# Kernel optimization log

Measured on AMD Instinct MI355X. Metric: run time of the kernel, lower is better.

The kernel has to match this reference:

```python
import jax, jax.numpy as jnp
import numpy as np

DMODEL = 1024
N_MAMBAS = 4
D_INNER = 2 * DMODEL          # expand = 2
D_STATE = 16                  # mamba_ssm default
D_CONV = 4                    # mamba_ssm default
DT_RANK = DMODEL // 16        # ceil(d_model/16) = 64


def setup_inputs() -> dict:
    key = jax.random.key(0)
    ks = jax.random.split(key, 8)
    B, L, n = 2, 4096, N_MAMBAS
    f32 = jnp.float32
    x = jax.random.normal(ks[0], (B, L, DMODEL), f32)
    in_w = jax.random.normal(ks[1], (n, 2 * D_INNER, DMODEL), f32) * 0.02
    conv_w = jax.random.normal(ks[2], (n, D_INNER, D_CONV), f32) * 0.1
    conv_b = jnp.zeros((n, D_INNER), f32)
    xproj_w = jax.random.normal(ks[3], (n, DT_RANK + 2 * D_STATE, D_INNER), f32) * 0.02
    dt_w = jax.random.normal(ks[4], (n, D_INNER, DT_RANK), f32) * 0.02
    # softplus-inverse of dt_init ~ 0.01 (mamba-style dt bias init)
    dt_b = jnp.log(jnp.expm1(jnp.full((n, D_INNER), 0.01, f32)))
    # S4D-real init: A_log = log(1..d_state)
    A_log = jnp.log(jnp.broadcast_to(jnp.arange(1, D_STATE + 1, dtype=f32), (n, D_INNER, D_STATE)))
    D_skip = jnp.ones((n, D_INNER), f32)
    out_w = jax.random.normal(ks[5], (n, DMODEL, D_INNER), f32) * 0.02
    return dict(x=x, in_w=in_w, conv_w=conv_w, conv_b=conv_b, xproj_w=xproj_w,
                dt_w=dt_w, dt_b=dt_b, A_log=A_log, D_skip=D_skip, out_w=out_w)


def _mamba(x, in_w, conv_w, conv_b, xproj_w, dt_w, dt_b, A_log, D_skip, out_w):
    # x: (B, Lc, D)
    Bb = x.shape[0]
    xz = jnp.einsum('bld,ed->ble', x, in_w)                 # (B, Lc, 2*D_INNER)
    xi, z = jnp.split(xz, 2, axis=-1)
    # causal depthwise conv over time
    xc = jnp.transpose(xi, (0, 2, 1))                       # (B, D_INNER, Lc)
    xc = jax.lax.conv_general_dilated(xc, conv_w[:, None, :], (1,),
                                      [(D_CONV - 1, 0)], feature_group_count=D_INNER)
    xi = jax.nn.silu(jnp.transpose(xc + conv_b[None, :, None], (0, 2, 1)))  # (B, Lc, D_INNER)
    proj = jnp.einsum('bld,ed->ble', xi, xproj_w)           # (B, Lc, DT_RANK + 2*D_STATE)
    dt = proj[..., :DT_RANK]
    Bm = proj[..., DT_RANK:DT_RANK + D_STATE]
    Cm = proj[..., DT_RANK + D_STATE:]
    dt = jax.nn.softplus(jnp.einsum('blr,dr->bld', dt, dt_w) + dt_b)  # (B, Lc, D_INNER)
    A = -jnp.exp(A_log)                                     # (D_INNER, D_STATE)

    def step(h, inp):
        dt_t, B_t, C_t, x_t = inp                           # (B,Di),(B,Ds),(B,Ds),(B,Di)
        dA = jnp.exp(dt_t[:, :, None] * A)                  # (B, Di, Ds)
        h = dA * h + dt_t[:, :, None] * B_t[:, None, :] * x_t[:, :, None]
        return h, jnp.einsum('bds,bs->bd', h, C_t)

    h0 = jnp.zeros((Bb, D_INNER, D_STATE), x.dtype)
    xs_t = (jnp.swapaxes(dt, 0, 1), jnp.swapaxes(Bm, 0, 1),
            jnp.swapaxes(Cm, 0, 1), jnp.swapaxes(xi, 0, 1))
    _, ys = jax.lax.scan(step, h0, xs_t)                    # (Lc, B, D_INNER)
    y = jnp.swapaxes(ys, 0, 1) + xi * D_skip                # (B, Lc, D_INNER)
    y = y * jax.nn.silu(z)
    return jnp.einsum('ble,de->bld', y, out_w)              # (B, Lc, D)


def reference(x, in_w, conv_w, conv_b, xproj_w, dt_w, dt_b, A_log, D_skip, out_w):
    B, L, D = x.shape
    n = N_MAMBAS
    # strided slices x[:, i::n] == reshape(B, L//n, n, D)[:, :, i]
    xs = jnp.transpose(x.reshape(B, L // n, n, D), (2, 0, 1, 3))   # (n, B, Lc, D)
    ys = jax.vmap(_mamba)(xs, in_w, conv_w, conv_b, xproj_w,
                          dt_w, dt_b, A_log, D_skip, out_w)        # (n, B, Lc, D)
    # torch.cat(dim=1) concatenates per-mamba outputs block-wise along seq
    return jnp.transpose(ys, (1, 0, 2, 3)).reshape(B, L, D)
```

## Files before the change

kernel.cpp:

```cpp
#include <hip/hip_runtime.h>
#include <math.h>

#define DM   1024
#define DI   2048
#define DSn  16
#define DTR  64
#define PW   96
#define LS   1024
#define NCH  16
#define CL   64
#define XKS  4

typedef unsigned short u16;
typedef unsigned int   u32;
typedef __attribute__((ext_vector_type(8))) short bf16x8;
typedef __attribute__((ext_vector_type(8))) unsigned short u16x8;
typedef __attribute__((ext_vector_type(4))) float f32x4;

__device__ __forceinline__ void bar_lds() {
  asm volatile("s_waitcnt lgkmcnt(0)\n\ts_barrier" ::: "memory");
}

__device__ __forceinline__ void split2(float f, u16& hi, u16& lo) {
  union { float f; unsigned int u; } v; v.f = f;
  hi = (u16)(v.u >> 16);
  union { unsigned int u; float f; } w; w.u = v.u & 0xffff0000u;
  union { float f; unsigned int u; } r; r.f = f - w.f;
  lo = (u16)(r.u >> 16);
}

template<int ROWS>
__device__ __forceinline__ bf16x8 frag(const u16* T, int l4, int row) {
  return *(const bf16x8*)&T[(l4 * ROWS + row) * 8];
}

template<int ROWS>
__device__ __forceinline__ void stage16f(const float* a, u16* Th, u16* Tl, int ra, int half) {
  #pragma unroll
  for (int q = 0; q < 2; ++q) {
    u16x8 vh, vl;
    #pragma unroll
    for (int c = 0; c < 8; ++c) {
      u16 h_, l_;
      split2(a[q * 8 + c], h_, l_);
      vh[c] = h_; vl[c] = l_;
    }
    const int slot = ((half * 2 + q) * ROWS + ra) * 8;
    *(u16x8*)&Th[slot] = vh;
    *(u16x8*)&Tl[slot] = vl;
  }
}

__global__ __launch_bounds__(256) void k_split_x(
    const float* __restrict__ x, u16* __restrict__ xh, u16* __restrict__ xl, int ib0)
{
  const int idx = blockIdx.x * 256 + threadIdx.x;
  const int t = idx >> 8, kq = (idx & 255) * 4;
  const int gt = ib0 * 1024 + t;
  const int j = gt & (LS - 1), ib = gt >> 10;
  const int i = ib >> 1, bb = ib & 1;
  const float4 v = *(const float4*)&x[(size_t)(bb * 4096 + j * 4 + i) * DM + kq];
  ushort4 vh, vl;
  split2(v.x, vh.x, vl.x); split2(v.y, vh.y, vl.y);
  split2(v.z, vh.z, vl.z); split2(v.w, vh.w, vl.w);
  *(ushort4*)&xh[(size_t)t * DM + kq] = vh;
  *(ushort4*)&xl[(size_t)t * DM + kq] = vl;
}

#define KGP 2064
__global__ __launch_bounds__(512, 2) void k_inproj(
    const u16* __restrict__ xh, const u16* __restrict__ xl,
    const float* __restrict__ inwf,
    float* __restrict__ xz, int ib0, int swz)
{
  __shared__ __align__(16) u16 L[2][4][4][KGP];
  const int tid = threadIdx.x;
  int mblk, nblk;
  if (swz) {
    const int o = blockIdx.x;
    const int xcd = o & 7, within = o >> 3;
    mblk = xcd * 4 + (within & 3);
    nblk = within >> 2;
  } else {
    mblk = blockIdx.x; nblk = blockIdx.y;
  }
  const int m0 = mblk << 8, n0 = nblk << 8;
  const int ib = ib0 + (m0 >> 10);
  const int il = (ib >> 1) - (ib0 >> 1);
  const int ra = tid >> 1, half = tid & 1;
  const u16* Aph = xh + (size_t)(m0 + ra) * DM + half * 16;
  const u16* Apl = xl + (size_t)(m0 + ra) * DM + half * 16;
  const float* Bpf = inwf + ((size_t)il * 4096 + n0 + ra) * DM + half * 16;
  const int w = tid >> 6, lane = tid & 63;
  const int wr = w >> 2, wc = w & 3;
  const int l15 = lane & 15, l4 = lane >> 4;

  f32x4 acc[8][4];
  #pragma unroll
  for (int a_ = 0; a_ < 8; ++a_)
    #pragma unroll
    for (int b_ = 0; b_ < 4; ++b_) acc[a_][b_] = (f32x4)(0.f);

  u16x8 ah2[2], al2[2];
  float br[16];

  auto LOADG = [&](int kt) {
    const int k0 = kt * 32;
    ah2[0] = *(const u16x8*)(Aph + k0);
    ah2[1] = *(const u16x8*)(Aph + k0 + 8);
    al2[0] = *(const u16x8*)(Apl + k0);
    al2[1] = *(const u16x8*)(Apl + k0 + 8);
    *(f32x4*)&br[0]  = *(const f32x4*)(Bpf + k0);
    *(f32x4*)&br[4]  = *(const f32x4*)(Bpf + k0 + 4);
    *(f32x4*)&br[8]  = *(const f32x4*)(Bpf + k0 + 8);
    *(f32x4*)&br[12] = *(const f32x4*)(Bpf + k0 + 12);
  };
  auto STORE = [&](int b) {
    #pragma unroll
    for (int q = 0; q < 2; ++q) {
      const int kg = half * 2 + q;
      *(u16x8*)&L[b][0][kg][ra * 8] = ah2[q];
      *(u16x8*)&L[b][1][kg][ra * 8] = al2[q];
      u16x8 vh, vl;
      #pragma unroll
      for (int c = 0; c < 8; ++c) {
        u16 h_, l_;
        split2(br[q * 8 + c], h_, l_);
        vh[c] = h_; vl[c] = l_;
      }
      *(u16x8*)&L[b][2][kg][ra * 8] = vh;
      *(u16x8*)&L[b][3][kg][ra * 8] = vl;
    }
  };
  auto COMPUTE = [&](int b) {
    bf16x8 bh[4], bl[4];
    #pragma unroll
    for (int nf = 0; nf < 4; ++nf) {
      const int col = wc * 64 + nf * 16 + l15;
      bh[nf] = *(const bf16x8*)&L[b][2][l4][col * 8];
      bl[nf] = *(const bf16x8*)&L[b][3][l4][col * 8];
    }
    #pragma unroll
    for (int mf = 0; mf < 8; ++mf) {
      const int row = wr * 128 + mf * 16 + l15;
      bf16x8 ah = *(const bf16x8*)&L[b][0][l4][row * 8];
      bf16x8 al = *(const bf16x8*)&L[b][1][l4][row * 8];
      #pragma unroll
      for (int nf = 0; nf < 4; ++nf) {
        acc[mf][nf] = __builtin_amdgcn_mfma_f32_16x16x32_bf16(ah, bh[nf], acc[mf][nf], 0, 0, 0);
        acc[mf][nf] = __builtin_amdgcn_mfma_f32_16x16x32_bf16(ah, bl[nf], acc[mf][nf], 0, 0, 0);
        acc[mf][nf] = __builtin_amdgcn_mfma_f32_16x16x32_bf16(al, bh[nf], acc[mf][nf], 0, 0, 0);
      }
    }
  };

  const int nk = DM / 32;
  LOADG(0);
  STORE(0);
  if (nk > 1) LOADG(1);
  bar_lds();
  for (int kt = 0; kt < nk; ++kt) {
    const int c = kt & 1;
    if (kt + 1 < nk) STORE(c ^ 1);
    if (kt + 2 < nk) LOADG(kt + 2);
    COMPUTE(c);
    bar_lds();
  }

  #pragma unroll
  for (int mf = 0; mf < 8; ++mf) {
    const int row = m0 + wr * 128 + mf * 16 + l4 * 4;
    #pragma unroll
    for (int nf = 0; nf < 4; ++nf) {
      const int col = n0 + wc * 64 + nf * 16 + l15;
      #pragma unroll
      for (int r = 0; r < 4; ++r)
        xz[(size_t)(row + r) * (2 * DI) + col] = acc[mf][nf][r];
    }
  }
}

__global__ __launch_bounds__(256) void k_conv(
    const float* __restrict__ xz, const float* __restrict__ convw,
    const float* __restrict__ convb, float* __restrict__ xib,
    int ib0, int ntok)
{
  const int idx = blockIdx.x * 256 + threadIdx.x;
  if (idx >= ntok * (DI / 4)) return;
  const int t = idx / (DI / 4);
  const int c = (idx - t * (DI / 4)) * 4;
  const int j = t & (LS - 1);
  const int i = (ib0 + (t >> 10)) >> 1;
  float4 acc = *(const float4*)&convb[(size_t)i * DI + c];
  float4 wt[4];
  #pragma unroll
  for (int q = 0; q < 4; ++q)
    wt[q] = *(const float4*)&convw[((size_t)i * DI + c + q) * 4];
  #pragma unroll
  for (int k = 0; k < 4; ++k) {
    const int j2 = j + k - 3;
    if (j2 >= 0) {
      const float4 v = *(const float4*)&xz[(size_t)(t + k - 3) * (2 * DI) + c];
      acc.x = fmaf(v.x, ((const float*)&wt[0])[k], acc.x);
      acc.y = fmaf(v.y, ((const float*)&wt[1])[k], acc.y);
      acc.z = fmaf(v.z, ((const float*)&wt[2])[k], acc.z);
      acc.w = fmaf(v.w, ((const float*)&wt[3])[k], acc.w);
    }
  }
  float4 o;
  o.x = acc.x / (1.f + __expf(-acc.x));
  o.y = acc.y / (1.f + __expf(-acc.y));
  o.z = acc.z / (1.f + __expf(-acc.z));
  o.w = acc.w / (1.f + __expf(-acc.w));
  *(float4*)&xib[(size_t)t * DI + c] = o;
}

__global__ __launch_bounds__(256) void k_xproj_part(
    const float* __restrict__ xif, const float* __restrict__ xwf,
    float* __restrict__ Pp, int ib0, int ntok)
{
  __shared__ __align__(16) u16 Ah[2][4*64*8], Al[2][4*64*8];
  __shared__ __align__(16) u16 Bh[2][4*96*8], Bl[2][4*96*8];
  const int tid = threadIdx.x;
  const int m0 = blockIdx.x << 6;
  const int ks = blockIdx.y;
  const int kbase = ks * (DI / XKS);
  const int ib = ib0 + (m0 >> 10);
  const int il = (ib >> 1) - (ib0 >> 1);
  const int ra = tid >> 1, half = tid & 1;
  const bool hasA = (tid < 128);
  const bool hasB = (tid < 192);
  const float* Apf = xif + (size_t)(m0 + ra) * DI + kbase + half * 16;
  const float* Bpf = xwf + ((size_t)il * PW + ra) * DI + kbase + half * 16;
  const int w = tid >> 6, lane = tid & 63;
  const int l15 = lane & 15, l4 = lane >> 4;

  f32x4 acc[6];
  #pragma unroll
  for (int b_ = 0; b_ < 6; ++b_) acc[b_] = (f32x4)(0.f);

  float ar[16], br[16];
  auto LOADAB = [&](int kt) {
    const int k0 = kt * 32;
    if (hasA) {
      #pragma unroll
      for (int q = 0; q < 4; ++q) *(f32x4*)&ar[q*4] = *(const f32x4*)(Apf + k0 + q*4);
    }
    if (hasB) {
      #pragma unroll
      for (int q = 0; q < 4; ++q) *(f32x4*)&br[q*4] = *(const f32x4*)(Bpf + k0 + q*4);
    }
  };
  auto STORE = [&](int b) {
    if (hasA) stage16f<64>(ar, Ah[b], Al[b], ra, half);
    if (hasB) stage16f<96>(br, Bh[b], Bl[b], ra, half);
  };
  auto COMPUTE = [&](int b) {
    const int arow = w * 16 + l15;
    bf16x8 ah = frag<64>(Ah[b], l4, arow);
    bf16x8 al = frag<64>(Al[b], l4, arow);
    #pragma unroll
    for (int nf = 0; nf < 6; ++nf) {
      const int col = nf * 16 + l15;
      bf16x8 bh = frag<96>(Bh[b], l4, col);
      bf16x8 bl = frag<96>(Bl[b], l4, col);
      acc[nf] = __builtin_amdgcn_mfma_f32_16x16x32_bf16(ah, bh, acc[nf], 0, 0, 0);
      acc[nf] = __builtin_amdgcn_mfma_f32_16x16x32_bf16(ah, bl, acc[nf], 0, 0, 0);
      acc[nf] = __builtin_amdgcn_mfma_f32_16x16x32_bf16(al, bh, acc[nf], 0, 0, 0);
    }
  };

  const int nk = (DI / XKS) / 32;
  LOADAB(0);
  STORE(0);
  LOADAB(1);
  bar_lds();
  for (int kt = 0; kt < nk; ++kt) {
    const int c = kt & 1;
    if (kt + 1 < nk) STORE(c ^ 1);
    if (kt + 2 < nk) LOADAB(kt + 2);
    COMPUTE(c);
    bar_lds();
  }

  float* outp = Pp + (size_t)ks * ntok * PW;
  const int row = m0 + w * 16 + l4 * 4;
  #pragma unroll
  for (int nf = 0; nf < 6; ++nf) {
    const int col = nf * 16 + l15;
    #pragma unroll
    for (int r = 0; r < 4; ++r)
      outp[(size_t)(row + r) * PW + col] = acc[nf][r];
  }
}

__global__ __launch_bounds__(256) void k_xproj_red(
    const float* __restrict__ Pp, float* __restrict__ projb, int ntok)
{
  const int idx = blockIdx.x * 256 + threadIdx.x;
  if (idx >= ntok * PW) return;
  const size_t plane = (size_t)ntok * PW;
  float s = 0.f;
  #pragma unroll
  for (int ks = 0; ks < XKS; ++ks) s += Pp[(size_t)ks * plane + idx];
  projb[idx] = s;
}

__global__ __launch_bounds__(256) void k_dtproj(
    const float* __restrict__ proj, const float* __restrict__ dtw,
    const float* __restrict__ dtbias, float* __restrict__ dtout,
    int dstride, int ib0)
{
  __shared__ __align__(16) u16 Ah[8*128*8], Al[8*128*8];
  __shared__ __align__(16) u16 Bh[8*128*8], Bl[8*128*8];
  const int tid = threadIdx.x;
  const int n0 = blockIdx.x << 7;
  const int m0 = blockIdx.y << 7;
  const int ib = ib0 + (m0 >> 10);
  const int i  = ib >> 1;
  const int ra = tid >> 1, half = tid & 1;
  const float* Ap = proj + (size_t)(m0 + ra) * PW + half * 32;
  const float* Bp = dtw + ((size_t)i * DI + n0 + ra) * DTR + half * 32;
  const int w = tid >> 6, lane = tid & 63;
  const int wr = w >> 1, wc = w & 1;
  const int l15 = lane & 15, l4 = lane >> 4;

  {
    float av[32], bv[32];
    #pragma unroll
    for (int q = 0; q < 8; ++q) *(f32x4*)&av[q*4] = *(const f32x4*)(Ap + q*4);
    #pragma unroll
    for (int q = 0; q < 8; ++q) *(f32x4*)&bv[q*4] = *(const f32x4*)(Bp + q*4);
    #pragma unroll
    for (int q = 0; q < 4; ++q) {
      u16x8 vh, vl, wh, wl;
      #pragma unroll
      for (int c = 0; c < 8; ++c) {
        u16 h_, l_;
        split2(av[q*8+c], h_, l_); vh[c] = h_; vl[c] = l_;
        split2(bv[q*8+c], h_, l_); wh[c] = h_; wl[c] = l_;
      }
      const int slot = ((half*4 + q) * 128 + ra) * 8;
      *(u16x8*)&Ah[slot] = vh; *(u16x8*)&Al[slot] = vl;
      *(u16x8*)&Bh[slot] = wh; *(u16x8*)&Bl[slot] = wl;
    }
  }
  __syncthreads();

  f32x4 acc[4][4];
  #pragma unroll
  for (int a_ = 0; a_ < 4; ++a_)
    #pragma unroll
    for (int b_ = 0; b_ < 4; ++b_) acc[a_][b_] = (f32x4)(0.f);

  #pragma unroll
  for (int c = 0; c < 2; ++c) {
    bf16x8 bh[4], bl[4];
    #pragma unroll
    for (int nf = 0; nf < 4; ++nf) {
      const int col = wc * 64 + nf * 16 + l15;
      bh[nf] = *(const bf16x8*)&Bh[((4*c + l4) * 128 + col) * 8];
      bl[nf] = *(const bf16x8*)&Bl[((4*c + l4) * 128 + col) * 8];
    }
    #pragma unroll
    for (int mf = 0; mf < 4; ++mf) {
      const int row = wr * 64 + mf * 16 + l15;
      bf16x8 ah = *(const bf16x8*)&Ah[((4*c + l4) * 128 + row) * 8];
      bf16x8 al = *(const bf16x8*)&Al[((4*c + l4) * 128 + row) * 8];
      #pragma unroll
      for (int nf = 0; nf < 4; ++nf) {
        acc[mf][nf] = __builtin_amdgcn_mfma_f32_16x16x32_bf16(ah, bh[nf], acc[mf][nf], 0, 0, 0);
        acc[mf][nf] = __builtin_amdgcn_mfma_f32_16x16x32_bf16(ah, bl[nf], acc[mf][nf], 0, 0, 0);
        acc[mf][nf] = __builtin_amdgcn_mfma_f32_16x16x32_bf16(al, bh[nf], acc[mf][nf], 0, 0, 0);
      }
    }
  }

  #pragma unroll
  for (int nf = 0; nf < 4; ++nf) {
    const int col = n0 + wc * 64 + nf * 16 + l15;
    const float bias = dtbias[(size_t)i * DI + col];
    #pragma unroll
    for (int mf = 0; mf < 4; ++mf) {
      const int t0 = m0 + wr * 64 + mf * 16 + l4 * 4;
      #pragma unroll
      for (int r = 0; r < 4; ++r) {
        const float u = acc[mf][nf][r] + bias;
        const float sp = (u > 20.f) ? u : log1pf(__expf(u));
        dtout[(size_t)(t0 + r) * dstride + col] = sp;
      }
    }
  }
}

__global__ __launch_bounds__(256) void k_scan_part(
    const float* __restrict__ projb, const float* dtp, int dstride,
    const float* __restrict__ xib, const float* __restrict__ A_log,
    float* __restrict__ Pbuf, float* __restrict__ Hbuf, int ib0)
{
  const int d = blockIdx.x * 256 + threadIdx.x;
  const int ch = blockIdx.y, lib = blockIdx.z;
  const int i = (ib0 + lib) >> 1;
  const size_t gd = (size_t)i * DI + d;
  __shared__ float bs[CL][DSn];
  const size_t trow = (size_t)lib * LS + (size_t)ch * CL;
  for (int p = threadIdx.x; p < CL * DSn; p += 256) {
    const int jj = p >> 4, ss = p & 15;
    bs[jj][ss] = projb[(trow + jj) * PW + DTR + ss];
  }
  float A[DSn], P[DSn], h[DSn];
  #pragma unroll
  for (int s = 0; s < DSn; ++s) {
    A[s] = -__expf(A_log[gd * DSn + s]);
    P[s] = 1.f; h[s] = 0.f;
  }
  __syncthreads();
  float dt_c = dtp[trow * dstride + d];
  float xi_c = xib[trow * DI + d];
  for (int j = 0; j < CL; ++j) {
    float dt_n = 0.f, xi_n = 0.f;
    if (j + 1 < CL) {
      dt_n = dtp[(trow + j + 1) * dstride + d];
      xi_n = xib[(trow + j + 1) * DI + d];
    }
    const float dx = dt_c * xi_c;
    #pragma unroll
    for (int s = 0; s < DSn; ++s) {
      const float dA = __expf(dt_c * A[s]);
      P[s] *= dA;
      h[s] = fmaf(dA, h[s], dx * bs[j][s]);
    }
    dt_c = dt_n; xi_c = xi_n;
  }
  const size_t base = ((size_t)(lib * NCH + ch) * DSn) * DI + d;
  #pragma unroll
  for (int s = 0; s < DSn; ++s) {
    Pbuf[base + (size_t)s * DI] = P[s];
    Hbuf[base + (size_t)s * DI] = h[s];
  }
}

__global__ __launch_bounds__(256) void k_scan_mid(
    float* __restrict__ Pbuf, const float* __restrict__ Hbuf, int nib)
{
  const int idx = blockIdx.x * 256 + threadIdx.x;
  if (idx >= nib * DSn * DI) return;
  const int d = idx & (DI - 1);
  const int s = (idx >> 11) & 15;
  const int lib = idx >> 15;
  const size_t stride = (size_t)DSn * DI;
  const size_t base = ((size_t)lib * NCH * DSn + s) * DI + d;
  float carry = 0.f;
  for (int c = 0; c < NCH; ++c) {
    const size_t o = base + (size_t)c * stride;
    const float p = Pbuf[o];
    const float hl = Hbuf[o];
    Pbuf[o] = carry;
    carry = fmaf(p, carry, hl);
  }
}

__global__ __launch_bounds__(256) void k_scan_full(
    const float* __restrict__ projb, const float* dtp, int dstride,
    float* xibio, const float* xzz,
    const float* __restrict__ A_log, const float* __restrict__ D_skip,
    const float* __restrict__ Pbuf, int ib0)
{
  const int d = blockIdx.x * 256 + threadIdx.x;
  const int ch = blockIdx.y, lib = blockIdx.z;
  const int i = (ib0 + lib) >> 1;
  const size_t gd = (size_t)i * DI + d;
  __shared__ float bs[CL][2 * DSn];
  const size_t trow = (size_t)lib * LS + (size_t)ch * CL;
  for (int p = threadIdx.x; p < CL * 2 * DSn; p += 256) {
    const int jj = p >> 5, ss = p & 31;
    bs[jj][ss] = projb[(trow + jj) * PW + DTR + ss];
  }
  float A[DSn], h[DSn];
  const size_t hbase = ((size_t)(lib * NCH + ch) * DSn) * DI + d;
  #pragma unroll
  for (int s = 0; s < DSn; ++s) {
    A[s] = -__expf(A_log[gd * DSn + s]);
    h[s] = Pbuf[hbase + (size_t)s * DI];
  }
  const float Dsk = D_skip[gd];
  __syncthreads();
  float dt_c = dtp[trow * dstride + d];
  float xi_c = xibio[trow * DI + d];
  float z_c  = xzz[trow * (2 * DI) + DI + d];
  for (int j = 0; j < CL; ++j) {
    float dt_n = 0.f, xi_n = 0.f, z_n = 0.f;
    if (j + 1 < CL) {
      dt_n = dtp[(trow + j + 1) * dstride + d];
      xi_n = xibio[(trow + j + 1) * DI + d];
      z_n  = xzz[(trow + j + 1) * (2 * DI) + DI + d];
    }
    const float dx = dt_c * xi_c;
    float y = 0.f;
    #pragma unroll
    for (int s = 0; s < DSn; ++s) {
      const float dA = __expf(dt_c * A[s]);
      h[s] = fmaf(dA, h[s], dx * bs[j][s]);
      y = fmaf(h[s], bs[j][DSn + s], y);
    }
    const float sz = z_c / (1.f + __expf(-z_c));
    const float val = (y + xi_c * Dsk) * sz;
    u16 vh, vl;
    split2(val, vh, vl);
    ((u32*)xibio)[(trow + j) * DI + d] = ((u32)vh << 16) | (u32)vl;
    dt_c = dt_n; xi_c = xi_n; z_c = z_n;
  }
}

__global__ __launch_bounds__(256) void k_outproj(
    const u32* __restrict__ ybp, const float* __restrict__ owf,
    float* __restrict__ out, int ib0)
{
  __shared__ __align__(16) u16 Ah[2][4*128*8], Al[2][4*128*8];
  __shared__ __align__(16) u16 Bh[2][4*128*8], Bl[2][4*128*8];
  const int tid = threadIdx.x;
  const int m0 = blockIdx.x << 7;
  const int n0 = blockIdx.y << 7;
  const int ib = ib0 + (m0 >> 10);
  const int i = ib >> 1, bb = ib & 1;
  const int il = i - (ib0 >> 1);
  const int ra = tid >> 1, half = tid & 1;
  const u32* Ap = ybp + (size_t)(m0 + ra) * DI + half * 16;
  const int rb = tid >> 1;
  const float* Bpf = owf + ((size_t)il * DM + n0 + rb) * DI + half * 16;
  const int w = tid >> 6, lane = tid & 63;
  const int wr = w >> 1, wc = w & 1;
  const int l15 = lane & 15, l4 = lane >> 4;

  f32x4 acc[4][4];
  #pragma unroll
  for (int a_ = 0; a_ < 4; ++a_)
    #pragma unroll
    for (int b_ = 0; b_ < 4; ++b_) acc[a_][b_] = (f32x4)(0.f);

  uint4 qa[4];
  float br[16];
  auto LOADG = [&](int kt) {
    const int k0 = kt * 32;
    qa[0] = *(const uint4*)(Ap + k0);     qa[1] = *(const uint4*)(Ap + k0 + 4);
    qa[2] = *(const uint4*)(Ap + k0 + 8); qa[3] = *(const uint4*)(Ap + k0 + 12);
    #pragma unroll
    for (int q = 0; q < 4; ++q) *(f32x4*)&br[q*4] = *(const f32x4*)(Bpf + k0 + q*4);
  };
  auto STORE = [&](int b) {
    #pragma unroll
    for (int g = 0; g < 2; ++g) {
      const u32 e[8] = { qa[2*g].x, qa[2*g].y, qa[2*g].z, qa[2*g].w,
                         qa[2*g+1].x, qa[2*g+1].y, qa[2*g+1].z, qa[2*g+1].w };
      u16x8 vh, vl;
      #pragma unroll
      for (int c = 0; c < 8; ++c) { vh[c] = (u16)(e[c] >> 16); vl[c] = (u16)(e[c] & 0xffffu); }
      const int slot = ((half*2+g)*128 + ra)*8;
      *(u16x8*)&Ah[b][slot] = vh;
      *(u16x8*)&Al[b][slot] = vl;
    }
    stage16f<128>(br, Bh[b], Bl[b], rb, half);
  };
  auto COMPUTE = [&](int b) {
    bf16x8 ah[4], al[4];
    #pragma unroll
    for (int mf = 0; mf < 4; ++mf) {
      const int row = wr * 64 + mf * 16 + l15;
      ah[mf] = frag<128>(Ah[b], l4, row);
      al[mf] = frag<128>(Al[b], l4, row);
    }
    #pragma unroll
    for (int nf = 0; nf < 4; ++nf) {
      const int col = wc * 64 + nf * 16 + l15;
      bf16x8 bh = frag<128>(Bh[b], l4, col);
      bf16x8 bl = frag<128>(Bl[b], l4, col);
      #pragma unroll
      for (int mf = 0; mf < 4; ++mf) {
        acc[mf][nf] = __builtin_amdgcn_mfma_f32_16x16x32_bf16(ah[mf], bh, acc[mf][nf], 0, 0, 0);
        acc[mf][nf] = __builtin_amdgcn_mfma_f32_16x16x32_bf16(ah[mf], bl, acc[mf][nf], 0, 0, 0);
        acc[mf][nf] = __builtin_amdgcn_mfma_f32_16x16x32_bf16(al[mf], bh, acc[mf][nf], 0, 0, 0);
      }
    }
  };

  const int nk = DI / 32;
  LOADG(0);
  STORE(0);
  LOADG(1);
  bar_lds();
  for (int kt = 0; kt < nk; ++kt) {
    const int c = kt & 1;
    if (kt + 1 < nk) STORE(c ^ 1);
    if (kt + 2 < nk) LOADG(kt + 2);
    COMPUTE(c);
    bar_lds();
  }

  #pragma unroll
  for (int mf = 0; mf < 4; ++mf) {
    const int t0 = m0 + wr * 64 + mf * 16 + l4 * 4;
    #pragma unroll
    for (int nf = 0; nf < 4; ++nf) {
      const int col = n0 + wc * 64 + nf * 16 + l15;
      #pragma unroll
      for (int r = 0; r < 4; ++r) {
        const int j = (t0 + r) & (LS - 1);
        out[(size_t)(bb * 4096 + i * 1024 + j) * DM + col] = acc[mf][nf][r];
      }
    }
  }
}

extern "C" void kernel_launch(void* const* d_in, const int* in_sizes, int n_in,
                              void* d_out, int out_size, void* d_ws, size_t ws_size,
                              hipStream_t stream) {
  (void)in_sizes; (void)n_in; (void)out_size;
  const float* x       = (const float*)d_in[0];
  const float* in_w    = (const float*)d_in[1];
  const float* conv_w  = (const float*)d_in[2];
  const float* conv_b  = (const float*)d_in[3];
  const float* xproj_w = (const float*)d_in[4];
  const float* dt_w    = (const float*)d_in[5];
  const float* dt_b    = (const float*)d_in[6];
  const float* A_log   = (const float*)d_in[7];
  const float* D_skip  = (const float*)d_in[8];
  const float* out_w   = (const float*)d_in[9];
  float* out = (float*)d_out;
  const dim3 blk(256);

  const size_t needSP = ((size_t)8192 * 4096 + (size_t)8192 * 2048 + (size_t)8192 * 96) * 4;
  if (ws_size >= needSP) {
    const size_t nt = 8192;
    float* xz    = (float*)d_ws;
    float* xib   = xz + nt * (2 * DI);
    float* projb = xib + nt * DI;
    u16* xph  = (u16*)d_out;  u16* xpl  = xph + nt * DM;
    float* Pp = (float*)d_out;
    float* Pbuf = (float*)d_out;
    float* Hbuf = Pbuf + (size_t)8 * NCH * DSn * DI;
    float* dtz = xz;
    u32* ybp  = (u32*)xib;

    k_split_x<<<dim3((int)nt), blk, 0, stream>>>(x, xph, xpl, 0);
    k_inproj<<<dim3(512), dim3(512), 0, stream>>>(xph, xpl, in_w, xz, 0, 1);
    k_conv<<<dim3((int)(nt*(DI/4)/256)), blk, 0, stream>>>(xz, conv_w, conv_b, xib, 0, (int)nt);
    k_xproj_part<<<dim3((int)(nt/64), XKS), blk, 0, stream>>>(xib, xproj_w, Pp, 0, (int)nt);
    k_xproj_red<<<dim3((int)(nt*PW/256)), blk, 0, stream>>>(Pp, projb, (int)nt);
    k_dtproj<<<dim3(DI/128, (int)(nt/128)), blk, 0, stream>>>(projb, dt_w, dt_b, dtz, 2*DI, 0);
    k_scan_part<<<dim3(DI/256, NCH, 8), blk, 0, stream>>>(projb, dtz, 2*DI, xib, A_log, Pbuf, Hbuf, 0);
    k_scan_mid<<<dim3(8 * DSn * DI / 256), blk, 0, stream>>>(Pbuf, Hbuf, 8);
    k_scan_full<<<dim3(DI/256, NCH, 8), blk, 0, stream>>>(projb, dtz, 2*DI, xib, xz, A_log, D_skip, Pbuf, 0);
    k_outproj<<<dim3((int)(nt/128), 8), blk, 0, stream>>>(ybp, out_w, out, 0);
    return;
  }

  auto needFB = [](int nib) -> size_t { return (size_t)nib * 29753344ull; };
  const int step = (ws_size >= needFB(4)) ? 4 : 2;

  for (int ib0 = 0; ib0 < 8; ib0 += step) {
    const int nib = step;
    const size_t nt = (size_t)nib * LS;
    const int i0 = ib0 >> 1;
    float* xz    = (float*)d_ws;
    float* xib   = xz + nt * (2 * DI);
    float* projb = xib + nt * DI;
    float* SH    = projb + nt * PW;
    u16* xph  = (u16*)SH;  u16* xpl = xph + nt * DM;
    float* Pp = SH;
    float* Pbuf = SH;
    float* Hbuf = Pbuf + (size_t)nib * NCH * DSn * DI / 2;
    float* dtz = xz;
    u32* ybp  = (u32*)xib;

    k_split_x<<<dim3((int)nt), blk, 0, stream>>>(x, xph, xpl, ib0);
    k_inproj<<<dim3((int)(nt/256), 16), dim3(512), 0, stream>>>(xph, xpl, in_w + (size_t)i0*4096*DM, xz, ib0, 0);
    k_conv<<<dim3((int)(nt*(DI/4)/256)), blk, 0, stream>>>(xz, conv_w, conv_b, xib, ib0, (int)nt);
    k_xproj_part<<<dim3((int)(nt/64), XKS), blk, 0, stream>>>(xib, xproj_w + (size_t)i0*PW*DI, Pp, ib0, (int)nt);
    k_xproj_red<<<dim3((int)(nt*PW/256)), blk, 0, stream>>>(Pp, projb, (int)nt);
    k_dtproj<<<dim3(DI/128, (int)(nt/128)), blk, 0, stream>>>(projb, dt_w, dt_b, dtz, 2*DI, ib0);
    k_scan_part<<<dim3(DI/256, NCH, nib), blk, 0, stream>>>(projb, dtz, 2*DI, xib, A_log, Pbuf, Hbuf, ib0);
    k_scan_mid<<<dim3(nib * DSn * DI / 256), blk, 0, stream>>>(Pbuf, Hbuf, nib);
    k_scan_full<<<dim3(DI/256, NCH, nib), blk, 0, stream>>>(projb, dtz, 2*DI, xib, xz, A_log, D_skip, Pbuf, ib0);
    k_outproj<<<dim3((int)(nt/128), 8), blk, 0, stream>>>(ybp, out_w + (size_t)i0*DM*DI, out, ib0);
  }
}
```

Baseline: 604.7 us.

## Shrink in-projection GEMM tile to 128x128 with single-buffered LDS

The in-projection GEMM block tile drops from 256x256 with 512 threads to 128x128 with 256 threads, and the grid grows to match. LDS goes from double-buffered to a single buffer with two barriers per k-step, and the XCD swizzle is adjusted for the new block count. The aim is more resident blocks per CU and better load balance across 2048 blocks. The cost is less data reuse per block, more global traffic for the operands, and an extra barrier each iteration.

```diff
diff --git a/kernel.cpp b/kernel.cpp
--- a/kernel.cpp
+++ b/kernel.cpp
@@ -67,24 +67,24 @@
   *(ushort4*)&xl[(size_t)t * DM + kq] = vl;
 }
 
-#define KGP 2064
-__global__ __launch_bounds__(512, 2) void k_inproj(
+#define KGQ 1040
+__global__ __launch_bounds__(256, 3) void k_inproj(
     const u16* __restrict__ xh, const u16* __restrict__ xl,
     const float* __restrict__ inwf,
     float* __restrict__ xz, int ib0, int swz)
 {
-  __shared__ __align__(16) u16 L[2][4][4][KGP];
+  __shared__ __align__(16) u16 Ah[4*KGQ], Al[4*KGQ], Bh[4*KGQ], Bl[4*KGQ];
   const int tid = threadIdx.x;
   int mblk, nblk;
   if (swz) {
     const int o = blockIdx.x;
     const int xcd = o & 7, within = o >> 3;
-    mblk = xcd * 4 + (within & 3);
-    nblk = within >> 2;
+    mblk = xcd * 8 + (within & 7);
+    nblk = within >> 3;
   } else {
     mblk = blockIdx.x; nblk = blockIdx.y;
   }
-  const int m0 = mblk << 8, n0 = nblk << 8;
+  const int m0 = mblk << 7, n0 = nblk << 7;
   const int ib = ib0 + (m0 >> 10);
   const int il = (ib >> 1) - (ib0 >> 1);
   const int ra = tid >> 1, half = tid & 1;
@@ -92,12 +92,12 @@
   const u16* Apl = xl + (size_t)(m0 + ra) * DM + half * 16;
   const float* Bpf = inwf + ((size_t)il * 4096 + n0 + ra) * DM + half * 16;
   const int w = tid >> 6, lane = tid & 63;
-  const int wr = w >> 2, wc = w & 3;
+  const int wr = w >> 1, wc = w & 1;
   const int l15 = lane & 15, l4 = lane >> 4;
 
-  f32x4 acc[8][4];
-  #pragma unroll
-  for (int a_ = 0; a_ < 8; ++a_)
+  f32x4 acc[4][4];
+  #pragma unroll
+  for (int a_ = 0; a_ < 4; ++a_)
     #pragma unroll
     for (int b_ = 0; b_ < 4; ++b_) acc[a_][b_] = (f32x4)(0.f);
 
@@ -115,12 +115,12 @@
     *(f32x4*)&br[8]  = *(const f32x4*)(Bpf + k0 + 8);
     *(f32x4*)&br[12] = *(const f32x4*)(Bpf + k0 + 12);
   };
-  auto STORE = [&](int b) {
+  auto STORE = [&]() {
     #pragma unroll
     for (int q = 0; q < 2; ++q) {
       const int kg = half * 2 + q;
-      *(u16x8*)&L[b][0][kg][ra * 8] = ah2[q];
-      *(u16x8*)&L[b][1][kg][ra * 8] = al2[q];
+      *(u16x8*)&Ah[kg * KGQ + ra * 8] = ah2[q];
+      *(u16x8*)&Al[kg * KGQ + ra * 8] = al2[q];
       u16x8 vh, vl;
       #pragma unroll
       for (int c = 0; c < 8; ++c) {
@@ -128,23 +128,23 @@
         split2(br[q * 8 + c], h_, l_);
         vh[c] = h_; vl[c] = l_;
       }
-      *(u16x8*)&L[b][2][kg][ra * 8] = vh;
-      *(u16x8*)&L[b][3][kg][ra * 8] = vl;
-    }
-  };
-  auto COMPUTE = [&](int b) {
+      *(u16x8*)&Bh[kg * KGQ + ra * 8] = vh;
+      *(u16x8*)&Bl[kg * KGQ + ra * 8] = vl;
+    }
+  };
+  auto COMPUTE = [&]() {
     bf16x8 bh[4], bl[4];
     #pragma unroll
     for (int nf = 0; nf < 4; ++nf) {
       const int col = wc * 64 + nf * 16 + l15;
-      bh[nf] = *(const bf16x8*)&L[b][2][l4][col * 8];
-      bl[nf] = *(const bf16x8*)&L[b][3][l4][col * 8];
-    }
-    #pragma unroll
-    for (int mf = 0; mf < 8; ++mf) {
-      const int row = wr * 128 + mf * 16 + l15;
-      bf16x8 ah = *(const bf16x8*)&L[b][0][l4][row * 8];
-      bf16x8 al = *(const bf16x8*)&L[b][1][l4][row * 8];
+      bh[nf] = *(const bf16x8*)&Bh[l4 * KGQ + col * 8];
+      bl[nf] = *(const bf16x8*)&Bl[l4 * KGQ + col * 8];
+    }
+    #pragma unroll
+    for (int mf = 0; mf < 4; ++mf) {
+      const int row = wr * 64 + mf * 16 + l15;
+      bf16x8 ah = *(const bf16x8*)&Ah[l4 * KGQ + row * 8];
+      bf16x8 al = *(const bf16x8*)&Al[l4 * KGQ + row * 8];
       #pragma unroll
       for (int nf = 0; nf < 4; ++nf) {
         acc[mf][nf] = __builtin_amdgcn_mfma_f32_16x16x32_bf16(ah, bh[nf], acc[mf][nf], 0, 0, 0);
@@ -156,20 +156,22 @@
 
   const int nk = DM / 32;
   LOADG(0);
-  STORE(0);
-  if (nk > 1) LOADG(1);
+  STORE();
   bar_lds();
+  LOADG(1);
   for (int kt = 0; kt < nk; ++kt) {
-    const int c = kt & 1;
-    if (kt + 1 < nk) STORE(c ^ 1);
-    if (kt + 2 < nk) LOADG(kt + 2);
-    COMPUTE(c);
-    bar_lds();
-  }
-
-  #pragma unroll
-  for (int mf = 0; mf < 8; ++mf) {
-    const int row = m0 + wr * 128 + mf * 16 + l4 * 4;
+    COMPUTE();
+    if (kt + 1 < nk) {
+      bar_lds();
+      STORE();
+      bar_lds();
+      if (kt + 2 < nk) LOADG(kt + 2);
+    }
+  }
+
+  #pragma unroll
+  for (int mf = 0; mf < 4; ++mf) {
+    const int row = m0 + wr * 64 + mf * 16 + l4 * 4;
     #pragma unroll
     for (int nf = 0; nf < 4; ++nf) {
       const int col = n0 + wc * 64 + nf * 16 + l15;
@@ -642,7 +644,7 @@
     u32* ybp  = (u32*)xib;
 
     k_split_x<<<dim3((int)nt), blk, 0, stream>>>(x, xph, xpl, 0);
-    k_inproj<<<dim3(512), dim3(512), 0, stream>>>(xph, xpl, in_w, xz, 0, 1);
+    k_inproj<<<dim3(2048), blk, 0, stream>>>(xph, xpl, in_w, xz, 0, 1);
     k_conv<<<dim3((int)(nt*(DI/4)/256)), blk, 0, stream>>>(xz, conv_w, conv_b, xib, 0, (int)nt);
     k_xproj_part<<<dim3((int)(nt/64), XKS), blk, 0, stream>>>(xib, xproj_w, Pp, 0, (int)nt);
     k_xproj_red<<<dim3((int)(nt*PW/256)), blk, 0, stream>>>(Pp, projb, (int)nt);
@@ -673,7 +675,7 @@
     u32* ybp  = (u32*)xib;
 
     k_split_x<<<dim3((int)nt), blk, 0, stream>>>(x, xph, xpl, ib0);
-    k_inproj<<<dim3((int)(nt/256), 16), dim3(512), 0, stream>>>(xph, xpl, in_w + (size_t)i0*4096*DM, xz, ib0, 0);
+    k_inproj<<<dim3((int)(nt/128), 32), blk, 0, stream>>>(xph, xpl, in_w + (size_t)i0*4096*DM, xz, ib0, 0);
     k_conv<<<dim3((int)(nt*(DI/4)/256)), blk, 0, stream>>>(xz, conv_w, conv_b, xib, ib0, (int)nt);
     k_xproj_part<<<dim3((int)(nt/64), XKS), blk, 0, stream>>>(xib, xproj_w + (size_t)i0*PW*DI, Pp, ib0, (int)nt);
     k_xproj_red<<<dim3((int)(nt*PW/256)), blk, 0, stream>>>(Pp, projb, (int)nt);
```

Result: slower. 632.9 us (+4.7%).
